# Kernel optimization log

Hardware: AMD Instinct MI355X
Metric: run time of the kernel (lower is better)

## Reference

```python
import jax, jax.numpy as jnp
import numpy as np

B, N, C, H = 16, 577, 768, 12
D = C // H
BETA = 1.0
KEEP_RATIO = 0.5


def setup_inputs() -> dict:
    key = jax.random.key(0)
    k0, k1, k2, k3 = jax.random.split(key, 4)
    x = jax.random.normal(k0, (B, N, C), dtype=jnp.float32)
    # UCB visit-count buffer, strictly positive as accumulated counts would be
    ucb_count_score = jax.random.uniform(k1, (H, N), dtype=jnp.float32) * 50.0 + 1.0
    Wqkv = jax.random.normal(k2, (3 * C, C), dtype=jnp.float32) * 0.02
    Wproj = jax.random.normal(k3, (C, C), dtype=jnp.float32) * 0.02
    bproj = jnp.zeros((C,), dtype=jnp.float32)
    counter = 60  # > 50 so pruning path is taken
    return {"x": x, "ucb_count_score": ucb_count_score, "Wqkv": Wqkv,
            "Wproj": Wproj, "bproj": bproj, "counter": counter}


def reference(x, ucb_count_score, Wqkv, Wproj, bproj, counter):
    # UCBAttention.forward with pruning_enabled=True, selection_mode='ucb',
    # ucb_update_enabled=True, exclude_cls=True, dropout=0 (eval).
    Bs, Ns, Cs = x.shape
    scale = D ** -0.5
    k_keep = max(1, int((Ns - 1) * KEEP_RATIO))  # _get_k with keep_ratio

    qkv = (x @ Wqkv.T).reshape(Bs, Ns, 3, H, D).transpose(2, 0, 3, 1, 4)  # [3,B,H,N,D]
    q, k, v = qkv[0], qkv[1], qkv[2]
    attn_scores = jnp.einsum('bhqd,bhkd->bhqk', q, k) * scale
    attn_probs = jax.nn.softmax(attn_scores, axis=-1)  # [B,H,N,N]

    # UCB scores over patches (CLS excluded)
    patch_scores = attn_probs[:, :, :, 1:].mean(axis=2)            # [B,H,N-1]
    expl = BETA * jnp.sqrt(jnp.log(counter + 1.0) / (ucb_count_score[:, 1:] + 1e-6))
    ucb_scores = patch_scores + expl[None, :, :]                   # [B,H,N-1]
    global_ucb = ucb_scores.mean(axis=1)                           # [B,N-1]
    _, topk_rel = jax.lax.top_k(global_ucb, k_keep)                # [B,k]
    kept = topk_rel + 1                                            # token indices

    # keep-vector: CLS (0) always kept; mask[i,j] = kept[i] OR kept[j]
    kv_mask = (jnp.zeros((Bs, Ns), attn_probs.dtype)
               .at[jnp.arange(Bs)[:, None], kept].set(1.0)
               .at[:, 0].set(1.0))                                 # [B,N]
    mask = jnp.maximum(kv_mask[:, None, :, None], kv_mask[:, None, None, :])  # [B,1,N,N]

    pruned = attn_probs * mask
    pruned = pruned / (pruned.sum(axis=-1, keepdims=True) + 1e-8)
    context = jnp.einsum('bhqk,bhkd->bhqd', pruned, v)             # [B,H,N,D]

    out = context.transpose(0, 2, 1, 3).reshape(Bs, Ns, Cs) @ Wproj.T + bproj

    # score_delta: +1/B at each kept token column, broadcast over heads
    delta = jnp.zeros((Ns,), jnp.float32).at[kept.reshape(-1)].add(1.0 / Bs)
    score_delta = jnp.broadcast_to(delta[None, :], ucb_count_score.shape)
    return out, score_delta, kept
```

## Files before the change

### kernel.cpp

```cpp
#include <hip/hip_runtime.h>
#include <cstdio>
#include <cstdint>

#define B_    16
#define N_    577
#define C_    768
#define H_    12
#define D_    64
#define KKEEP 288
#define SCALE 0.125f
#define LOG2E 1.4426950408889634f
#define M_TOT (B_ * N_)
#define NKT   24
#define PLROW ((size_t)N_ * 64)

typedef __bf16 bf16x8_t __attribute__((ext_vector_type(8)));
typedef __bf16 bf16x4_t __attribute__((ext_vector_type(4)));
typedef float  f32x4_t  __attribute__((ext_vector_type(4)));
typedef unsigned int u32x4_t __attribute__((ext_vector_type(4)));
typedef unsigned int u32x2_t __attribute__((ext_vector_type(2)));

__device__ __forceinline__ f32x4_t mfma_bf16(bf16x8_t a, bf16x8_t b, f32x4_t c) {
    return __builtin_amdgcn_mfma_f32_16x16x32_bf16(a, b, c, 0, 0, 0);
}

__device__ __forceinline__ void gload16(const ushort* g, ushort* l) {
    __builtin_amdgcn_global_load_lds(
        (const __attribute__((address_space(1))) void*)g,
        (__attribute__((address_space(3))) void*)l, 16, 0, 0);
}
#define VMCNT(n) asm volatile("s_waitcnt vmcnt(" #n ")" ::: "memory")
#define LGKM0()  asm volatile("s_waitcnt lgkmcnt(0)" ::: "memory")
#define SB() __builtin_amdgcn_sched_barrier(0)

__device__ __forceinline__ int xcd_swz(int bid, int nwg) {
    int q = nwg >> 3, r = nwg & 7;
    int xcd = bid & 7, off = bid >> 3;
    int base = (xcd < r) ? xcd * (q + 1) : r * (q + 1) + (xcd - r) * q;
    return base + off;
}

__device__ __forceinline__ void splitf(float x, unsigned int &hi, unsigned int &lo) {
    unsigned int u = __float_as_uint(x);
    hi = u >> 16;
    float r = x - __uint_as_float(u & 0xffff0000u);
    lo = __float_as_uint(r) >> 16;
}
__device__ __forceinline__ unsigned int bf16rne(float x) {
    unsigned int u = __float_as_uint(x);
    return (u + 0x7fffu + ((u >> 16) & 1u)) >> 16;
}

__device__ __forceinline__ void pack_tile(const float* __restrict__ src,
                                          ushort* __restrict__ dH,
                                          ushort* __restrict__ dL,
                                          int nrows, int tile) {
    int kt = tile % NKT, mt = tile / NKT;
    int w = threadIdx.x;
    int row = w >> 1, h = w & 1;
    int m = mt * 128 + row;
    int sw = (row >> 1) & 3;
    float f[16];
    if (m < nrows) {
        const float* s = src + (size_t)m * C_ + kt * 32;
        int sa = (2 * h) ^ sw, sb = (2 * h + 1) ^ sw;
        *(float4*)&f[0]  = *(const float4*)(s + sa * 8);
        *(float4*)&f[4]  = *(const float4*)(s + sa * 8 + 4);
        *(float4*)&f[8]  = *(const float4*)(s + sb * 8);
        *(float4*)&f[12] = *(const float4*)(s + sb * 8 + 4);
    } else {
#pragma unroll
        for (int i = 0; i < 16; i++) f[i] = 0.f;
    }
    unsigned hi[16], lo[16];
#pragma unroll
    for (int i = 0; i < 16; i++) splitf(f[i], hi[i], lo[i]);
    u32x4_t h0 = {hi[0] | (hi[1] << 16), hi[2] | (hi[3] << 16),
                  hi[4] | (hi[5] << 16), hi[6] | (hi[7] << 16)};
    u32x4_t h1 = {hi[8] | (hi[9] << 16), hi[10] | (hi[11] << 16),
                  hi[12] | (hi[13] << 16), hi[14] | (hi[15] << 16)};
    u32x4_t l0 = {lo[0] | (lo[1] << 16), lo[2] | (lo[3] << 16),
                  lo[4] | (lo[5] << 16), lo[6] | (lo[7] << 16)};
    u32x4_t l1 = {lo[8] | (lo[9] << 16), lo[10] | (lo[11] << 16),
                  lo[12] | (lo[13] << 16), lo[14] | (lo[15] << 16)};
    size_t dbase = (size_t)tile * 4096 + row * 32;
    *(u32x4_t*)&dH[dbase + (2 * h) * 8]     = h0;
    *(u32x4_t*)&dH[dbase + (2 * h + 1) * 8] = h1;
    *(u32x4_t*)&dL[dbase + (2 * h) * 8]     = l0;
    *(u32x4_t*)&dL[dbase + (2 * h + 1) * 8] = l1;
}

__device__ __forceinline__ void pack_tile_rne(const float* __restrict__ src,
                                              ushort* __restrict__ dst,
                                              int nrows, int tile) {
    int kt = tile % NKT, mt = tile / NKT;
    int w = threadIdx.x;
    int row = w >> 1, h = w & 1;
    int m = mt * 128 + row;
    int sw = (row >> 1) & 3;
    float f[16];
    if (m < nrows) {
        const float* s = src + (size_t)m * C_ + kt * 32;
        int sa = (2 * h) ^ sw, sb = (2 * h + 1) ^ sw;
        *(float4*)&f[0]  = *(const float4*)(s + sa * 8);
        *(float4*)&f[4]  = *(const float4*)(s + sa * 8 + 4);
        *(float4*)&f[8]  = *(const float4*)(s + sb * 8);
        *(float4*)&f[12] = *(const float4*)(s + sb * 8 + 4);
    } else {
#pragma unroll
        for (int i = 0; i < 16; i++) f[i] = 0.f;
    }
    unsigned hi[16];
#pragma unroll
    for (int i = 0; i < 16; i++) hi[i] = bf16rne(f[i]);
    u32x4_t h0 = {hi[0] | (hi[1] << 16), hi[2] | (hi[3] << 16),
                  hi[4] | (hi[5] << 16), hi[6] | (hi[7] << 16)};
    u32x4_t h1 = {hi[8] | (hi[9] << 16), hi[10] | (hi[11] << 16),
                  hi[12] | (hi[13] << 16), hi[14] | (hi[15] << 16)};
    size_t dbase = (size_t)tile * 4096 + row * 32;
    *(u32x4_t*)&dst[dbase + (2 * h) * 8]     = h0;
    *(u32x4_t*)&dst[dbase + (2 * h + 1) * 8] = h1;
}

#define NXP 1752
#define NWP 432
#define NPJ 144
#define NZ  37

__global__ __launch_bounds__(256) void pack_all_kernel(const float* __restrict__ x,
                                                       const float* __restrict__ Wqkv,
                                                       const float* __restrict__ Wproj,
                                                       ushort* __restrict__ XplH,
                                                       ushort* __restrict__ XplL,
                                                       ushort* __restrict__ WplH,
                                                       ushort* __restrict__ WplL,
                                                       ushort* __restrict__ Wpjb,
                                                       float* __restrict__ kvmask) {
    int bid = blockIdx.x;
    if (bid < NXP) {
        pack_tile(x, XplH, XplL, M_TOT, bid);
    } else if (bid < NXP + NWP) {
        pack_tile(Wqkv, WplH, WplL, 3 * C_, bid - NXP);
    } else if (bid < NXP + NWP + NPJ) {
        pack_tile_rne(Wproj, Wpjb, C_, bid - NXP - NWP);
    } else {
        int i = (bid - NXP - NWP - NPJ) * 256 + threadIdx.x;
        if (i < B_ * N_) kvmask[i] = 0.f;
    }
}

__device__ __forceinline__ bf16x8_t fragT(const ushort* H, int row, int c, int ls) {
    int phys = ((c << 2) + ls) ^ (row & 7);
    return __builtin_bit_cast(bf16x8_t, *(const u32x4_t*)&H[(row << 6) + (phys << 3)]);
}

__global__ __launch_bounds__(256) void gemm_qkv_mfma(const ushort* __restrict__ XplH,
                                                     const ushort* __restrict__ XplL,
                                                     const ushort* __restrict__ WplH,
                                                     const ushort* __restrict__ WplL,
                                                     ushort* __restrict__ qhp,
                                                     ushort* __restrict__ qlp,
                                                     ushort* __restrict__ khp,
                                                     ushort* __restrict__ klp,
                                                     ushort* __restrict__ vtp) {
    __shared__ ushort SMEM[32768];
    ushort* Ah = SMEM;
    ushort* Al = SMEM + 8192;
    ushort* Bh = SMEM + 16384;
    ushort* Bl = SMEM + 24576;
    const int bid = xcd_swz(blockIdx.x, 18 * 73);
    const int bx = bid % 18, by = bid / 18;
    const int tid = threadIdx.x;
    const int lane = tid & 63, wave = tid >> 6;
    const int wr = wave >> 1, wc = wave & 1;
    const int lr = lane & 15, ls = lane >> 4;
    const int m0 = by * 128;
    const int o0 = wave * 1024, o1 = o0 + 512;
    const int la = lane * 8;
    const size_t abase = (size_t)by * NKT * 4096;
    const size_t bbase = (size_t)bx * NKT * 4096;
    f32x4_t acc[4][4] = {};

    if (bx < 12) {
        auto stage = [&](int buf, int kt) {
            const size_t ta = abase + (size_t)kt * 4096;
            const size_t tb = bbase + (size_t)kt * 4096;
            gload16(XplH + ta + o0 + la, &Ah[buf * 4096 + o0]);
            gload16(XplH + ta + o1 + la, &Ah[buf * 4096 + o1]);
            gload16(XplL + ta + o0 + la, &Al[buf * 4096 + o0]);
            gload16(XplL + ta + o1 + la, &Al[buf * 4096 + o1]);
            gload16(WplH + tb + o0 + la, &Bh[buf * 4096 + o0]);
            gload16(WplH + tb + o1 + la, &Bh[buf * 4096 + o1]);
            gload16(WplL + tb + o0 + la, &Bl[buf * 4096 + o0]);
            gload16(WplL + tb + o1 + la, &Bl[buf * 4096 + o1]);
        };
        stage(0, 0);
#pragma unroll 1
        for (int kt = 0; kt < NKT; ++kt) {
            const int cur = kt & 1;
            if (kt + 1 < NKT) {
                stage(cur ^ 1, kt + 1);
                VMCNT(8);
            } else {
                VMCNT(0);
            }
            SB();
            __builtin_amdgcn_s_barrier();
            SB();
            bf16x8_t fah[4], fal[4], fbh[4], fbl[4];
#pragma unroll
            for (int i = 0; i < 4; i++) {
                int rowA = wr * 64 + i * 16 + lr;
                int pa = ls ^ ((rowA >> 1) & 3);
                fah[i] = __builtin_bit_cast(bf16x8_t, *(const u32x4_t*)&Ah[cur * 4096 + rowA * 32 + pa * 8]);
                fal[i] = __builtin_bit_cast(bf16x8_t, *(const u32x4_t*)&Al[cur * 4096 + rowA * 32 + pa * 8]);
                int rowB = wc * 64 + i * 16 + lr;
                int pb = ls ^ ((rowB >> 1) & 3);
                fbh[i] = __builtin_bit_cast(bf16x8_t, *(const u32x4_t*)&Bh[cur * 4096 + rowB * 32 + pb * 8]);
                fbl[i] = __builtin_bit_cast(bf16x8_t, *(const u32x4_t*)&Bl[cur * 4096 + rowB * 32 + pb * 8]);
            }
#pragma unroll
            for (int i = 0; i < 4; i++)
#pragma unroll
                for (int j = 0; j < 4; j++) {
                    acc[i][j] = mfma_bf16(fah[i], fbh[j], acc[i][j]);
                    acc[i][j] = mfma_bf16(fah[i], fbl[j], acc[i][j]);
                    acc[i][j] = mfma_bf16(fal[i], fbh[j], acc[i][j]);
                }
            if (kt + 1 < NKT) {
                SB();
                __builtin_amdgcn_s_barrier();
            }
        }
        const int n0 = bx * 128;
        const int s = n0 / C_;
        __syncthreads();
        unsigned* T = (unsigned*)SMEM;
        const float sc = (s == 0) ? SCALE * LOG2E : 1.0f;
#pragma unroll
        for (int j = 0; j < 4; j++) {
            int nl = wc * 64 + j * 16 + lr;
#pragma unroll
            for (int i = 0; i < 4; i++) {
#pragma unroll
                for (int r = 0; r < 4; r++) {
                    int ml = wr * 64 + i * 16 + ls * 4 + r;
                    unsigned hi, lo;
                    splitf(acc[i][j][r] * sc, hi, lo);
                    int idx = ml * 128 + ((((nl >> 3) ^ ((ml >> 2) & 7)) << 3) | (nl & 7));
                    T[idx] = hi | (lo << 16);
                }
            }
        }
        __syncthreads();
        ushort* dh = (s == 1) ? khp : qhp;
        ushort* dl = (s == 1) ? klp : qlp;
        const int hh0 = (n0 % C_) / D_;
#pragma unroll
        for (int it = 0; it < 8; ++it) {
            int g = it * 256 + tid;
            int sl = g & 7;
            int m_local = (g >> 3) & 127;
            int hh_half = g >> 10;
            int m = m0 + m_local;
            if (m < M_TOT) {
                int b = m / N_, n = m % N_;
                int dg = sl ^ (n & 7);
                int grp = (hh_half * 8 + dg) ^ ((m_local >> 2) & 7);
                const unsigned* src = &T[m_local * 128 + grp * 8];
                u32x4_t a = *(const u32x4_t*)src;
                u32x4_t bvv = *(const u32x4_t*)(src + 4);
                u32x4_t hiv = {(a[0] & 0xffffu) | (a[1] << 16),
                               (a[2] & 0xffffu) | (a[3] << 16),
                               (bvv[0] & 0xffffu) | (bvv[1] << 16),
                               (bvv[2] & 0xffffu) | (bvv[3] << 16)};
                u32x4_t lov = {(a[0] >> 16) | (a[1] & 0xffff0000u),
                               (a[2] >> 16) | (a[3] & 0xffff0000u),
                               (bvv[0] >> 16) | (bvv[1] & 0xffff0000u),
                               (bvv[2] >> 16) | (bvv[3] & 0xffff0000u)};
                size_t off = (size_t)(b * H_ + hh0 + hh_half) * PLROW + (size_t)n * 64 + sl * 8;
                *(u32x4_t*)&dh[off] = hiv;
                *(u32x4_t*)&dl[off] = lov;
            }
        }
    } else {
        auto stage = [&](int buf, int kt) {
            const size_t ta = abase + (size_t)kt * 4096;
            const size_t tb = bbase + (size_t)kt * 4096;
            gload16(XplH + ta + o0 + la, &Ah[buf * 4096 + o0]);
            gload16(XplH + ta + o1 + la, &Ah[buf * 4096 + o1]);
            gload16(XplL + ta + o0 + la, &Al[buf * 4096 + o0]);
            gload16(XplL + ta + o1 + la, &Al[buf * 4096 + o1]);
            gload16(WplH + tb + o0 + la, &Bh[buf * 4096 + o0]);
            gload16(WplH + tb + o1 + la, &Bh[buf * 4096 + o1]);
        };
        stage(0, 0);
#pragma unroll 1
        for (int kt = 0; kt < NKT; ++kt) {
            const int cur = kt & 1;
            if (kt + 1 < NKT) {
                stage(cur ^ 1, kt + 1);
                VMCNT(6);
            } else {
                VMCNT(0);
            }
            SB();
            __builtin_amdgcn_s_barrier();
            SB();
            bf16x8_t fah[4], fal[4], fbh[4];
#pragma unroll
            for (int i = 0; i < 4; i++) {
                int rowA = wr * 64 + i * 16 + lr;
                int pa = ls ^ ((rowA >> 1) & 3);
                fah[i] = __builtin_bit_cast(bf16x8_t, *(const u32x4_t*)&Ah[cur * 4096 + rowA * 32 + pa * 8]);
                fal[i] = __builtin_bit_cast(bf16x8_t, *(const u32x4_t*)&Al[cur * 4096 + rowA * 32 + pa * 8]);
                int rowB = wc * 64 + i * 16 + lr;
                int pb = ls ^ ((rowB >> 1) & 3);
                fbh[i] = __builtin_bit_cast(bf16x8_t, *(const u32x4_t*)&Bh[cur * 4096 + rowB * 32 + pb * 8]);
            }
#pragma unroll
            for (int i = 0; i < 4; i++)
#pragma unroll
                for (int j = 0; j < 4; j++) {
                    acc[i][j] = mfma_bf16(fah[i], fbh[j], acc[i][j]);
                    acc[i][j] = mfma_bf16(fal[i], fbh[j], acc[i][j]);
                }
            if (kt + 1 < NKT) {
                SB();
                __builtin_amdgcn_s_barrier();
            }
        }
        const int n0v = (bx - 12) * 128;
#pragma unroll
        for (int j = 0; j < 4; j++) {
            int ng = n0v + wc * 64 + j * 16 + lr;
            int hh = ng / D_;
            int d = ng % D_;
#pragma unroll
            for (int i = 0; i < 4; i++) {
                int mg0 = m0 + wr * 64 + i * 16 + ls * 4;
#pragma unroll
                for (int r = 0; r < 4; r++) {
                    int m = mg0 + r;
                    if (m < M_TOT) {
                        int b = m / N_, n = m % N_;
                        int jt = n >> 6, jl = n & 63;
                        size_t off = ((size_t)(b * H_ + hh) * 10 + jt) * 4096 +
                                     (size_t)d * 64 + (((jl >> 3) ^ (d & 7)) << 3) + (jl & 7);
                        vtp[off] = __builtin_bit_cast(unsigned short, (__bf16)acc[i][j][r]);
                    }
                }
            }
        }
    }
}

__global__ __launch_bounds__(512) void attn_rowsum_mfma(const ushort* __restrict__ qh,
                                                        const ushort* __restrict__ ql,
                                                        const ushort* __restrict__ kh,
                                                        const ushort* __restrict__ kl,
                                                        float* __restrict__ w) {
    __shared__ ushort Qh[8192], Ql[8192];
    __shared__ ushort Kh[4096], Kl[4096];
    __shared__ float red[8][64];
    const int bid = xcd_swz(blockIdx.x, 5 * B_ * H_);
    const int bh = bid / 5, q0 = (bid % 5) * 128;
    const int tid = threadIdx.x, lane = tid & 63, wv = tid >> 6;
    const int wg = wv >> 2, wl = wv & 3;
    const int lr = lane & 15, ls = lane >> 4;
    const size_t bho = (size_t)bh * PLROW;
    const ushort* qhp = qh + bho; const ushort* qlp = ql + bho;
    const ushort* khp = kh + bho; const ushort* klp = kl + bho;
    auto qrow = [&](int rr) { return (size_t)min(q0 + wv * 16 + rr * 8 + (lane >> 3), N_ - 1) * 64 + (lane & 7) * 8; };
    gload16(qhp + qrow(0), &Qh[wv * 1024]);
    gload16(qhp + qrow(1), &Qh[wv * 1024 + 512]);
    gload16(qlp + qrow(0), &Ql[wv * 1024]);
    gload16(qlp + qrow(1), &Ql[wv * 1024 + 512]);
    auto krow = [&](int j0) { return (size_t)min(j0 + wv * 8 + (lane >> 3), N_ - 1) * 64 + (lane & 7) * 8; };
    auto stageK = [&](int j0) {
        gload16(khp + krow(j0), &Kh[wv * 512]);
        gload16(klp + krow(j0), &Kl[wv * 512]);
    };
    stageK(0);
    VMCNT(0);
    __syncthreads();
    bf16x8_t fqh[4][2], fql[4][2];
#pragma unroll
    for (int i = 0; i < 4; i++)
#pragma unroll
        for (int c = 0; c < 2; c++) {
            fqh[i][c] = fragT(Qh, wg * 64 + i * 16 + lr, c, ls);
            fql[i][c] = fragT(Ql, wg * 64 + i * 16 + lr, c, ls);
        }
    float rs[4] = {0.f, 0.f, 0.f, 0.f};
#pragma unroll 1
    for (int t = 0; t < 10; ++t) {
        bf16x8_t fkh[2], fkl[2];
#pragma unroll
        for (int c = 0; c < 2; c++) {
            fkh[c] = fragT(Kh, wl * 16 + lr, c, ls);
            fkl[c] = fragT(Kl, wl * 16 + lr, c, ls);
        }
        LGKM0(); SB();
        __builtin_amdgcn_s_barrier();
        SB();
        if (t < 9) stageK((t + 1) * 64);
        int jbase = t * 64 + wl * 16 + ls * 4;
#pragma unroll
        for (int i = 0; i < 4; i++) {
            f32x4_t s = {0.f, 0.f, 0.f, 0.f};
            __builtin_amdgcn_s_setprio(1);
#pragma unroll
            for (int c = 0; c < 2; c++) {
                s = mfma_bf16(fkh[c], fqh[i][c], s);
                s = mfma_bf16(fkh[c], fql[i][c], s);
                s = mfma_bf16(fkl[c], fqh[i][c], s);
            }
            __builtin_amdgcn_s_setprio(0);
#pragma unroll
            for (int r = 0; r < 4; r++)
                rs[i] += (jbase + r < N_) ? __builtin_amdgcn_exp2f(s[r]) : 0.f;
        }
        if (t < 9) {
            VMCNT(0); SB();
            __builtin_amdgcn_s_barrier();
            SB();
        }
    }
#pragma unroll
    for (int i = 0; i < 4; i++) {
        float v2 = rs[i];
        v2 += __shfl_xor(v2, 16);
        v2 += __shfl_xor(v2, 32);
        if (ls == 0) red[wv][i * 16 + lr] = v2;
    }
    __syncthreads();
    if (tid < 128) {
        int grp = tid >> 6, qlc = tid & 63;
        float s = red[grp * 4 + 0][qlc] + red[grp * 4 + 1][qlc] +
                  red[grp * 4 + 2][qlc] + red[grp * 4 + 3][qlc];
        int qn = q0 + tid;
        if (qn < N_) w[(size_t)bh * N_ + qn] = 1.0f / s;
    }
}

__global__ __launch_bounds__(512) void attn_colsum_mfma(const ushort* __restrict__ qh,
                                                        const ushort* __restrict__ ql,
                                                        const ushort* __restrict__ kh,
                                                        const ushort* __restrict__ kl,
                                                        const float* __restrict__ w,
                                                        float* __restrict__ colsum) {
    __shared__ ushort KhS[8192], KlS[8192];
    __shared__ ushort Qh[4096], Ql[4096];
    __shared__ float wsAll[640];
    __shared__ float red[8][64];
    const int bid = xcd_swz(blockIdx.x, 5 * B_ * H_);
    const int bh = bid / 5, j0 = (bid % 5) * 128;
    const int tid = threadIdx.x, lane = tid & 63, wv = tid >> 6;
    const int wg = wv >> 2, wl = wv & 3;
    const int lr = lane & 15, ls = lane >> 4;
    const size_t bho = (size_t)bh * PLROW;
    const ushort* qhp = qh + bho; const ushort* qlp = ql + bho;
    const ushort* khp = kh + bho; const ushort* klp = kl + bho;
    auto krow = [&](int rr) { return (size_t)min(j0 + wv * 16 + rr * 8 + (lane >> 3), N_ - 1) * 64 + (lane & 7) * 8; };
    gload16(khp + krow(0), &KhS[wv * 1024]);
    gload16(khp + krow(1), &KhS[wv * 1024 + 512]);
    gload16(klp + krow(0), &KlS[wv * 1024]);
    gload16(klp + krow(1), &KlS[wv * 1024 + 512]);
    auto qrow2 = [&](int qt) { return (size_t)min(qt + wv * 8 + (lane >> 3), N_ - 1) * 64 + (lane & 7) * 8; };
    auto stageQ = [&](int qt) {
        gload16(qhp + qrow2(qt), &Qh[wv * 512]);
        gload16(qlp + qrow2(qt), &Ql[wv * 512]);
    };
    stageQ(0);
    for (int i2 = tid; i2 < 640; i2 += 512)
        wsAll[i2] = (i2 < N_) ? w[(size_t)bh * N_ + i2] : 0.f;
    VMCNT(0);
    __syncthreads();
    bf16x8_t fkh[4][2], fkl[4][2];
#pragma unroll
    for (int i = 0; i < 4; i++)
#pragma unroll
        for (int c = 0; c < 2; c++) {
            fkh[i][c] = fragT(KhS, wg * 64 + i * 16 + lr, c, ls);
            fkl[i][c] = fragT(KlS, wg * 64 + i * 16 + lr, c, ls);
        }
    float cs[4] = {0.f, 0.f, 0.f, 0.f};
#pragma unroll 1
    for (int t = 0; t < 10; ++t) {
        bf16x8_t fqh[2], fql[2];
#pragma unroll
        for (int c = 0; c < 2; c++) {
            fqh[c] = fragT(Qh, wl * 16 + lr, c, ls);
            fql[c] = fragT(Ql, wl * 16 + lr, c, ls);
        }
        float wq[4];
#pragma unroll
        for (int r = 0; r < 4; r++) wq[r] = wsAll[t * 64 + wl * 16 + ls * 4 + r];
        LGKM0(); SB();
        __builtin_amdgcn_s_barrier();
        SB();
        if (t < 9) stageQ((t + 1) * 64);
#pragma unroll
        for (int i = 0; i < 4; i++) {
            f32x4_t s = {0.f, 0.f, 0.f, 0.f};
            __builtin_amdgcn_s_setprio(1);
#pragma unroll
            for (int c = 0; c < 2; c++) {
                s = mfma_bf16(fqh[c], fkh[i][c], s);
                s = mfma_bf16(fql[c], fkh[i][c], s);
                s = mfma_bf16(fqh[c], fkl[i][c], s);
            }
            __builtin_amdgcn_s_setprio(0);
#pragma unroll
            for (int r = 0; r < 4; r++) cs[i] += __builtin_amdgcn_exp2f(s[r]) * wq[r];
        }
        if (t < 9) {
            VMCNT(0); SB();
            __builtin_amdgcn_s_barrier();
            SB();
        }
    }
#pragma unroll
    for (int i = 0; i < 4; i++) {
        float v2 = cs[i];
        v2 += __shfl_xor(v2, 16);
        v2 += __shfl_xor(v2, 32);
        if (ls == 0) red[wv][i * 16 + lr] = v2;
    }
    __syncthreads();
    if (tid < 128) {
        int grp = tid >> 6, jlc = tid & 63;
        float t2 = red[grp * 4 + 0][jlc] + red[grp * 4 + 1][jlc] +
                   red[grp * 4 + 2][jlc] + red[grp * 4 + 3][jlc];
        int jn = j0 + tid;
        if (jn < N_) colsum[(size_t)bh * N_ + jn] = t2;
    }
}

__global__ __launch_bounds__(512) void topk_kernel(const float* __restrict__ colsum,
                                                   const float* __restrict__ ucb_count,
                                                   const int* __restrict__ counter,
                                                   float* __restrict__ kept_out,
                                                   float* __restrict__ kvmask) {
    __shared__ float sv[1024];
    __shared__ int si[1024];
    int b = blockIdx.x, tid = threadIdx.x;
    float lc = logf((float)counter[0] + 1.0f);
    for (int t = tid; t < 1024; t += 512) {
        if (t < N_ - 1) {
            int tok = t + 1;
            float accv = 0.f;
#pragma unroll
            for (int h = 0; h < H_; h++) {
                float csv = colsum[(size_t)(b * H_ + h) * N_ + tok];
                float patch = csv * (1.0f / (float)N_);
                float cnt = ucb_count[h * N_ + tok];
                float expl = sqrtf(lc / (cnt + 1e-6f));
                accv += patch + expl;
            }
            sv[t] = accv * (1.0f / (float)H_);
            si[t] = t;
        } else {
            sv[t] = -INFINITY;
            si[t] = 1 << 20;
        }
    }
    __syncthreads();
    for (int kk = 2; kk <= 1024; kk <<= 1) {
        for (int jj = kk >> 1; jj > 0; jj >>= 1) {
            for (int t = tid; t < 1024; t += 512) {
                int ixj = t ^ jj;
                if (ixj > t) {
                    float v1 = sv[t], v2 = sv[ixj];
                    int i1 = si[t], i2 = si[ixj];
                    bool before21 = (v2 > v1) || (v2 == v1 && i2 < i1);
                    bool dirDesc = ((t & kk) == 0);
                    if (before21 == dirDesc) {
                        sv[t] = v2; sv[ixj] = v1;
                        si[t] = i2; si[ixj] = i1;
                    }
                }
            }
            __syncthreads();
        }
    }
    for (int r = tid; r < KKEEP; r += 512) {
        int tok = si[r] + 1;
        kept_out[b * KKEEP + r] = (float)tok;
        kvmask[b * N_ + tok] = 1.0f;
    }
    if (tid == 0) kvmask[b * N_] = 1.0f;
}

__global__ __launch_bounds__(512) void attn_ctx_mfma(const ushort* __restrict__ qh,
                                                     const ushort* __restrict__ ql,
                                                     const ushort* __restrict__ kh,
                                                     const ushort* __restrict__ vtp,
                                                     const float* __restrict__ kvmask,
                                                     ushort* __restrict__ ctxb,
                                                     float* __restrict__ sd) {
    if (blockIdx.x >= 5 * B_ * H_) {
        int idx = (blockIdx.x - 5 * B_ * H_) * 512 + threadIdx.x;
        if (idx < H_ * N_) {
            int n = idx % N_;
            float d = 0.f;
            if (n != 0) {
#pragma unroll
                for (int b = 0; b < B_; b++) d += kvmask[b * N_ + n];
            }
            sd[idx] = d * (1.0f / (float)B_);
        }
        return;
    }
    __shared__ ushort Kh[2][4096], Vt[2][4096];
    __shared__ ushort Pl[2][4096];
    __shared__ float mkAll[640];
    float (*red)[64] = (float(*)[64])&Pl[0][0];
    float* inv = (float*)&Pl[1][0];
    const int bid = xcd_swz(blockIdx.x, 5 * B_ * H_);
    const int bh = bid / 5, q0 = (bid % 5) * 128;
    const int b = bh / H_, h = bh % H_;
    const int tid = threadIdx.x, lane = tid & 63, wv = tid >> 6;
    const int wg = wv >> 2, wl = wv & 3;
    const int lr = lane & 15, ls = lane >> 4;
    const size_t bho = (size_t)bh * PLROW;
    const ushort* qhp = qh + bho; const ushort* qlp = ql + bho;
    const ushort* khp = kh + bho;
    const ushort* vtb = vtp + (size_t)bh * 10 * 4096;
    ushort* PlS = &Pl[0][0];
    for (int i2 = tid; i2 < 640; i2 += 512)
        mkAll[i2] = (i2 < N_) ? kvmask[(size_t)b * N_ + i2] : 0.f;
    auto qrow = [&](int rr) { return (size_t)min(q0 + wv * 16 + rr * 8 + (lane >> 3), N_ - 1) * 64 + (lane & 7) * 8; };
    bf16x8_t fqh[4][2], fql[4][2];
    gload16(qhp + qrow(0), &PlS[wv * 1024]);
    gload16(qhp + qrow(1), &PlS[wv * 1024 + 512]);
    VMCNT(0); __syncthreads();
#pragma unroll
    for (int i = 0; i < 4; i++)
#pragma unroll
        for (int c = 0; c < 2; c++)
            fqh[i][c] = fragT(PlS, wg * 64 + i * 16 + lr, c, ls);
    __syncthreads();
    gload16(qlp + qrow(0), &PlS[wv * 1024]);
    gload16(qlp + qrow(1), &PlS[wv * 1024 + 512]);
    VMCNT(0); __syncthreads();
#pragma unroll
    for (int i = 0; i < 4; i++)
#pragma unroll
        for (int c = 0; c < 2; c++)
            fql[i][c] = fragT(PlS, wg * 64 + i * 16 + lr, c, ls);
    __syncthreads();
    auto krow = [&](int j0) { return (size_t)min(j0 + wv * 8 + (lane >> 3), N_ - 1) * 64 + (lane & 7) * 8; };
    auto stageKV = [&](int buf, int t) {
        gload16(khp + krow(t * 64), &Kh[buf][wv * 512]);
        gload16(vtb + (size_t)t * 4096 + wv * 512 + lane * 8, &Vt[buf][wv * 512]);
    };
    float mq[4];
#pragma unroll
    for (int i = 0; i < 4; i++) mq[i] = mkAll[q0 + wg * 64 + i * 16 + lr];
    stageKV(0, 0);
    f32x4_t acc[4] = {};
    float psums[4] = {0.f, 0.f, 0.f, 0.f};
#pragma unroll 1
    for (int t = 0; t < 10; ++t) {
        const int cur = t & 1;
        if (t < 9) { stageKV(cur ^ 1, t + 1); VMCNT(2); }
        else      { VMCNT(0); }
        SB(); __builtin_amdgcn_s_barrier(); SB();
        bf16x8_t fkh[2];
#pragma unroll
        for (int c = 0; c < 2; c++)
            fkh[c] = fragT(Kh[cur], wl * 16 + lr, c, ls);
        int jloc = wl * 16 + ls * 4;
        float jmv[4], jbias[4];
#pragma unroll
        for (int r = 0; r < 4; r++) {
            int j = t * 64 + jloc + r;
            jmv[r] = mkAll[t * 64 + jloc + r];
            jbias[r] = (j < N_) ? 0.f : -16384.f;
        }
#pragma unroll
        for (int i = 0; i < 4; i++) {
            f32x4_t s = {0.f, 0.f, 0.f, 0.f};
            __builtin_amdgcn_s_setprio(1);
#pragma unroll
            for (int c = 0; c < 2; c++) {
                s = mfma_bf16(fkh[c], fqh[i][c], s);
                s = mfma_bf16(fkh[c], fql[i][c], s);
            }
            __builtin_amdgcn_s_setprio(0);
            bf16x4_t pb;
            float mqi = mq[i];
#pragma unroll
            for (int r = 0; r < 4; r++) {
                float p = __builtin_amdgcn_exp2f(s[r] + jbias[r]) * fmaxf(mqi, jmv[r]);
                psums[i] += p;
                pb[r] = (__bf16)p;
            }
            int row = i * 16 + lr;
            int slot = ((wl << 1) + (ls >> 1)) ^ (row & 7);
            *(u32x2_t*)&Pl[wg][(row << 6) + (slot << 3) + ((ls & 1) << 2)] =
                __builtin_bit_cast(u32x2_t, pb);
        }
        SB(); LGKM0(); SB();
        __builtin_amdgcn_s_barrier();
        SB();
        bf16x8_t fv[2];
#pragma unroll
        for (int c = 0; c < 2; c++) fv[c] = fragT(Vt[cur], wl * 16 + lr, c, ls);
        __builtin_amdgcn_s_setprio(1);
#pragma unroll
        for (int i = 0; i < 4; i++) {
            bf16x8_t fp0 = fragT(Pl[wg], i * 16 + lr, 0, ls);
            bf16x8_t fp1 = fragT(Pl[wg], i * 16 + lr, 1, ls);
            acc[i] = mfma_bf16(fv[0], fp0, acc[i]);
            acc[i] = mfma_bf16(fv[1], fp1, acc[i]);
        }
        __builtin_amdgcn_s_setprio(0);
        if (t < 9) { SB(); __builtin_amdgcn_s_barrier(); }
    }
    __syncthreads();
#pragma unroll
    for (int i = 0; i < 4; i++) {
        float v2 = psums[i];
        v2 += __shfl_xor(v2, 16);
        v2 += __shfl_xor(v2, 32);
        if (ls == 0) red[wv][i * 16 + lr] = v2;
    }
    __syncthreads();
    if (tid < 128) {
        int grp = tid >> 6, qlc = tid & 63;
        float t2 = red[grp * 4 + 0][qlc] + red[grp * 4 + 1][qlc] +
                   red[grp * 4 + 2][qlc] + red[grp * 4 + 3][qlc];
        inv[tid] = 1.0f / (t2 + 1e-8f);
    }
    __syncthreads();
#pragma unroll
    for (int i = 0; i < 4; i++) {
        int qn = q0 + wg * 64 + i * 16 + lr;
        if (qn < N_) {
            float rn = inv[wg * 64 + i * 16 + lr];
            bf16x4_t ov;
            ov[0] = (__bf16)(acc[i][0] * rn);
            ov[1] = (__bf16)(acc[i][1] * rn);
            ov[2] = (__bf16)(acc[i][2] * rn);
            ov[3] = (__bf16)(acc[i][3] * rn);
            int m = b * N_ + qn;
            int col = h * D_ + wl * 16 + ls * 4;
            int mt = m >> 7, rowl = m & 127;
            int kt2 = col >> 5, c32 = col & 31;
            int phys = (c32 >> 3) ^ ((rowl >> 1) & 3);
            size_t off = ((size_t)(mt * NKT + kt2)) * 4096 + rowl * 32 + phys * 8 + (c32 & 7);
            *(u32x2_t*)&ctxb[off] = __builtin_bit_cast(u32x2_t, ov);
        }
    }
}

__global__ __launch_bounds__(256) void gemm_proj_mfma(const ushort* __restrict__ Apl,
                                                      const ushort* __restrict__ Bpl,
                                                      const float* __restrict__ bias,
                                                      float* __restrict__ out) {
    __shared__ ushort Ab[2][4096], Bb[2][4096];
    const int bid = xcd_swz(blockIdx.x, 6 * 73);
    const int bx = bid % 6, by = bid / 6;
    const int tid = threadIdx.x;
    const int lane = tid & 63, wave = tid >> 6;
    const int wr = wave >> 1, wc = wave & 1;
    const int lr = lane & 15, ls = lane >> 4;
    const int m0 = by * 128, n0 = bx * 128;
    const int o0 = wave * 1024, o1 = o0 + 512;
    const int la = lane * 8;
    const size_t abase = (size_t)by * NKT * 4096;
    const size_t bbase = (size_t)bx * NKT * 4096;
    f32x4_t acc[4][4] = {};

    auto stage = [&](int buf, int kt) {
        const size_t ta = abase + (size_t)kt * 4096;
        const size_t tb = bbase + (size_t)kt * 4096;
        gload16(Apl + ta + o0 + la, &Ab[buf][o0]);
        gload16(Apl + ta + o1 + la, &Ab[buf][o1]);
        gload16(Bpl + tb + o0 + la, &Bb[buf][o0]);
        gload16(Bpl + tb + o1 + la, &Bb[buf][o1]);
    };
    stage(0, 0);
#pragma unroll 1
    for (int kt = 0; kt < NKT; ++kt) {
        const int cur = kt & 1;
        if (kt + 1 < NKT) {
            stage(cur ^ 1, kt + 1);
            VMCNT(4);
        } else {
            VMCNT(0);
        }
        SB();
        __builtin_amdgcn_s_barrier();
        SB();
        bf16x8_t fa[4], fb[4];
#pragma unroll
        for (int i = 0; i < 4; i++) {
            int rowA = wr * 64 + i * 16 + lr;
            int pa = ls ^ ((rowA >> 1) & 3);
            fa[i] = __builtin_bit_cast(bf16x8_t, *(const u32x4_t*)&Ab[cur][rowA * 32 + pa * 8]);
            int rowB = wc * 64 + i * 16 + lr;
            int pb = ls ^ ((rowB >> 1) & 3);
            fb[i] = __builtin_bit_cast(bf16x8_t, *(const u32x4_t*)&Bb[cur][rowB * 32 + pb * 8]);
        }
#pragma unroll
        for (int i = 0; i < 4; i++)
#pragma unroll
            for (int j = 0; j < 4; j++)
                acc[i][j] = mfma_bf16(fa[i], fb[j], acc[i][j]);
        if (kt + 1 < NKT) {
            SB();
            __builtin_amdgcn_s_barrier();
        }
    }
#pragma unroll
    for (int j = 0; j < 4; j++) {
        int ng = n0 + wc * 64 + j * 16 + lr;
        float bb = bias[ng];
#pragma unroll
        for (int i = 0; i < 4; i++) {
            int mg0 = m0 + wr * 64 + i * 16 + ls * 4;
#pragma unroll
            for (int r = 0; r < 4; r++) {
                int m = mg0 + r;
                if (m < M_TOT) out[(size_t)m * C_ + ng] = acc[i][j][r] + bb;
            }
        }
    }
}

extern "C" void kernel_launch(void* const* d_in, const int* in_sizes, int n_in,
                              void* d_out, int out_size, void* d_ws, size_t ws_size,
                              hipStream_t stream) {
    const float* x     = (const float*)d_in[0];
    const float* ucb   = (const float*)d_in[1];
    const float* Wqkv  = (const float*)d_in[2];
    const float* Wproj = (const float*)d_in[3];
    const float* bproj = (const float*)d_in[4];
    const int*   counter = (const int*)d_in[5];

    const size_t BHN  = (size_t)B_ * H_ * N_;
    const size_t XPL  = (size_t)(73 * 128) * C_;
    const size_t WPL  = (size_t)3 * C_ * C_;
    const size_t WPJ  = (size_t)C_ * C_;
    const size_t PLN  = (size_t)192 * PLROW;
    const size_t VTSZ = (size_t)192 * 10 * 4096;

    ushort* qhp  = (ushort*)d_ws;
    ushort* qlp  = qhp + PLN;
    ushort* khp  = qlp + PLN;
    ushort* klp  = khp + PLN;
    ushort* vtp  = klp + PLN;
    ushort* XplH = vtp + VTSZ;
    ushort* XplL = XplH + XPL;
    ushort* ctxb = XplH;
    ushort* WplH = XplL + XPL;
    ushort* WplL = WplH + WPL;
    ushort* Wpjb = WplL + WPL;
    float*  w    = (float*)(Wpjb + WPJ);
    float*  colsum = w + BHN;
    float*  kvmask = colsum + BHN;
    size_t need = ((char*)(kvmask + (size_t)B_ * N_)) - (char*)d_ws;
    if (ws_size < need) {
        fprintf(stderr, "kernel_launch: ws too small, need %zu have %zu\n",
                need, ws_size);
        return;
    }

    float* out  = (float*)d_out;
    float* sd   = out + (size_t)B_ * N_ * C_;
    float* kept = sd + (size_t)H_ * N_;

    pack_all_kernel<<<NXP + NWP + NPJ + NZ, 256, 0, stream>>>(
        x, Wqkv, Wproj, XplH, XplL, WplH, WplL, Wpjb, kvmask);

    gemm_qkv_mfma<<<18 * 73, 256, 0, stream>>>(XplH, XplL, WplH, WplL,
                                               qhp, qlp, khp, klp, vtp);
    attn_rowsum_mfma<<<5 * B_ * H_, 512, 0, stream>>>(qhp, qlp, khp, klp, w);
    attn_colsum_mfma<<<5 * B_ * H_, 512, 0, stream>>>(qhp, qlp, khp, klp, w, colsum);
    topk_kernel<<<B_, 512, 0, stream>>>(colsum, ucb, counter, kept, kvmask);
    attn_ctx_mfma<<<5 * B_ * H_ + 14, 512, 0, stream>>>(qhp, qlp, khp, vtp,
                                                        kvmask, ctxb, sd);
    gemm_proj_mfma<<<6 * 73, 256, 0, stream>>>(ctxb, Wpjb, bproj, out);
}
```

Baseline: 282.6 us.

## Single-buffer QKV GEMM and attention KV tiles to cut LDS usage

Removes double-buffering of the A/B tiles in the QKV projection GEMM, halving its shared memory from 64KB to 32KB. The epilogue now writes hi and lo halves in two rounds through a 16-bit staging buffer. In the attention kernel, the K and V^T tiles are single-buffered too: fragments are read into registers first, then the next tile is prefetched while compute proceeds. The aim is more resident blocks per CU, at the cost of losing load/compute overlap in the GEMM, which now waits on VMCNT(0) every k-step.

```diff
diff --git a/kernel.cpp b/kernel.cpp
--- a/kernel.cpp
+++ b/kernel.cpp
@@ -163,11 +163,11 @@
                                                      ushort* __restrict__ khp,
                                                      ushort* __restrict__ klp,
                                                      ushort* __restrict__ vtp) {
-    __shared__ ushort SMEM[32768];
+    __shared__ ushort SMEM[16384];
     ushort* Ah = SMEM;
-    ushort* Al = SMEM + 8192;
-    ushort* Bh = SMEM + 16384;
-    ushort* Bl = SMEM + 24576;
+    ushort* Al = SMEM + 4096;
+    ushort* Bh = SMEM + 8192;
+    ushort* Bl = SMEM + 12288;
     const int bid = xcd_swz(blockIdx.x, 18 * 73);
     const int bx = bid % 18, by = bid / 18;
     const int tid = threadIdx.x;
@@ -175,35 +175,29 @@
     const int wr = wave >> 1, wc = wave & 1;
     const int lr = lane & 15, ls = lane >> 4;
     const int m0 = by * 128;
-    const int o0 = wave * 1024, o1 = o0 + 512;
+    const int ow = wave * 1024;
     const int la = lane * 8;
     const size_t abase = (size_t)by * NKT * 4096;
     const size_t bbase = (size_t)bx * NKT * 4096;
     f32x4_t acc[4][4] = {};
 
     if (bx < 12) {
-        auto stage = [&](int buf, int kt) {
+        auto stage = [&](int kt) {
             const size_t ta = abase + (size_t)kt * 4096;
             const size_t tb = bbase + (size_t)kt * 4096;
-            gload16(XplH + ta + o0 + la, &Ah[buf * 4096 + o0]);
-            gload16(XplH + ta + o1 + la, &Ah[buf * 4096 + o1]);
-            gload16(XplL + ta + o0 + la, &Al[buf * 4096 + o0]);
-            gload16(XplL + ta + o1 + la, &Al[buf * 4096 + o1]);
-            gload16(WplH + tb + o0 + la, &Bh[buf * 4096 + o0]);
-            gload16(WplH + tb + o1 + la, &Bh[buf * 4096 + o1]);
-            gload16(WplL + tb + o0 + la, &Bl[buf * 4096 + o0]);
-            gload16(WplL + tb + o1 + la, &Bl[buf * 4096 + o1]);
+            gload16(XplH + ta + ow + la, &Ah[ow]);
+            gload16(XplH + ta + ow + 512 + la, &Ah[ow + 512]);
+            gload16(XplL + ta + ow + la, &Al[ow]);
+            gload16(XplL + ta + ow + 512 + la, &Al[ow + 512]);
+            gload16(WplH + tb + ow + la, &Bh[ow]);
+            gload16(WplH + tb + ow + 512 + la, &Bh[ow + 512]);
+            gload16(WplL + tb + ow + la, &Bl[ow]);
+            gload16(WplL + tb + ow + 512 + la, &Bl[ow + 512]);
         };
-        stage(0, 0);
 #pragma unroll 1
         for (int kt = 0; kt < NKT; ++kt) {
-            const int cur = kt & 1;
-            if (kt + 1 < NKT) {
-                stage(cur ^ 1, kt + 1);
-                VMCNT(8);
-            } else {
-                VMCNT(0);
-            }
+            stage(kt);
+            VMCNT(0);
             SB();
             __builtin_amdgcn_s_barrier();
             SB();
@@ -212,12 +206,12 @@
             for (int i = 0; i < 4; i++) {
                 int rowA = wr * 64 + i * 16 + lr;
                 int pa = ls ^ ((rowA >> 1) & 3);
-                fah[i] = __builtin_bit_cast(bf16x8_t, *(const u32x4_t*)&Ah[cur * 4096 + rowA * 32 + pa * 8]);
-                fal[i] = __builtin_bit_cast(bf16x8_t, *(const u32x4_t*)&Al[cur * 4096 + rowA * 32 + pa * 8]);
+                fah[i] = __builtin_bit_cast(bf16x8_t, *(const u32x4_t*)&Ah[rowA * 32 + pa * 8]);
+                fal[i] = __builtin_bit_cast(bf16x8_t, *(const u32x4_t*)&Al[rowA * 32 + pa * 8]);
                 int rowB = wc * 64 + i * 16 + lr;
                 int pb = ls ^ ((rowB >> 1) & 3);
-                fbh[i] = __builtin_bit_cast(bf16x8_t, *(const u32x4_t*)&Bh[cur * 4096 + rowB * 32 + pb * 8]);
-                fbl[i] = __builtin_bit_cast(bf16x8_t, *(const u32x4_t*)&Bl[cur * 4096 + rowB * 32 + pb * 8]);
+                fbh[i] = __builtin_bit_cast(bf16x8_t, *(const u32x4_t*)&Bh[rowB * 32 + pb * 8]);
+                fbl[i] = __builtin_bit_cast(bf16x8_t, *(const u32x4_t*)&Bl[rowB * 32 + pb * 8]);
             }
 #pragma unroll
             for (int i = 0; i < 4; i++)
@@ -227,83 +221,68 @@
                     acc[i][j] = mfma_bf16(fah[i], fbl[j], acc[i][j]);
                     acc[i][j] = mfma_bf16(fal[i], fbh[j], acc[i][j]);
                 }
-            if (kt + 1 < NKT) {
-                SB();
-                __builtin_amdgcn_s_barrier();
-            }
+            SB();
+            __builtin_amdgcn_s_barrier();
         }
         const int n0 = bx * 128;
         const int s = n0 / C_;
-        __syncthreads();
-        unsigned* T = (unsigned*)SMEM;
         const float sc = (s == 0) ? SCALE * LOG2E : 1.0f;
-#pragma unroll
-        for (int j = 0; j < 4; j++) {
-            int nl = wc * 64 + j * 16 + lr;
-#pragma unroll
-            for (int i = 0; i < 4; i++) {
-#pragma unroll
-                for (int r = 0; r < 4; r++) {
-                    int ml = wr * 64 + i * 16 + ls * 4 + r;
-                    unsigned hi, lo;
-                    splitf(acc[i][j][r] * sc, hi, lo);
-                    int idx = ml * 128 + ((((nl >> 3) ^ ((ml >> 2) & 7)) << 3) | (nl & 7));
-                    T[idx] = hi | (lo << 16);
-                }
-            }
-        }
-        __syncthreads();
         ushort* dh = (s == 1) ? khp : qhp;
         ushort* dl = (s == 1) ? klp : qlp;
         const int hh0 = (n0 % C_) / D_;
-#pragma unroll
-        for (int it = 0; it < 8; ++it) {
-            int g = it * 256 + tid;
-            int sl = g & 7;
-            int m_local = (g >> 3) & 127;
-            int hh_half = g >> 10;
-            int m = m0 + m_local;
-            if (m < M_TOT) {
-                int b = m / N_, n = m % N_;
-                int dg = sl ^ (n & 7);
-                int grp = (hh_half * 8 + dg) ^ ((m_local >> 2) & 7);
-                const unsigned* src = &T[m_local * 128 + grp * 8];
-                u32x4_t a = *(const u32x4_t*)src;
-                u32x4_t bvv = *(const u32x4_t*)(src + 4);
-                u32x4_t hiv = {(a[0] & 0xffffu) | (a[1] << 16),
-                               (a[2] & 0xffffu) | (a[3] << 16),
-                               (bvv[0] & 0xffffu) | (bvv[1] << 16),
-                               (bvv[2] & 0xffffu) | (bvv[3] << 16)};
-                u32x4_t lov = {(a[0] >> 16) | (a[1] & 0xffff0000u),
-                               (a[2] >> 16) | (a[3] & 0xffff0000u),
-                               (bvv[0] >> 16) | (bvv[1] & 0xffff0000u),
-                               (bvv[2] >> 16) | (bvv[3] & 0xffff0000u)};
-                size_t off = (size_t)(b * H_ + hh0 + hh_half) * PLROW + (size_t)n * 64 + sl * 8;
-                *(u32x4_t*)&dh[off] = hiv;
-                *(u32x4_t*)&dl[off] = lov;
-            }
+        ushort* T16 = SMEM;
+#pragma unroll 1
+        for (int round = 0; round < 2; ++round) {
+#pragma unroll
+            for (int j = 0; j < 4; j++) {
+                int nl = wc * 64 + j * 16 + lr;
+#pragma unroll
+                for (int i = 0; i < 4; i++) {
+#pragma unroll
+                    for (int r = 0; r < 4; r++) {
+                        int ml = wr * 64 + i * 16 + ls * 4 + r;
+                        unsigned hi, lo;
+                        splitf(acc[i][j][r] * sc, hi, lo);
+                        int idx = ml * 128 + ((((nl >> 3) ^ ((ml >> 2) & 7)) << 3) | (nl & 7));
+                        T16[idx] = (ushort)(round ? lo : hi);
+                    }
+                }
+            }
+            __syncthreads();
+            ushort* dst = round ? dl : dh;
+#pragma unroll
+            for (int it = 0; it < 8; ++it) {
+                int g = it * 256 + tid;
+                int sl = g & 7;
+                int m_local = (g >> 3) & 127;
+                int hh_half = g >> 10;
+                int m = m0 + m_local;
+                if (m < M_TOT) {
+                    int b = m / N_, n = m % N_;
+                    int dg = sl ^ (n & 7);
+                    int grp = (hh_half * 8 + dg) ^ ((m_local >> 2) & 7);
+                    u32x4_t vv = *(const u32x4_t*)&T16[m_local * 128 + grp * 8];
+                    size_t off = (size_t)(b * H_ + hh0 + hh_half) * PLROW + (size_t)n * 64 + sl * 8;
+                    *(u32x4_t*)&dst[off] = vv;
+                }
+            }
+            if (round == 0) __syncthreads();
         }
     } else {
-        auto stage = [&](int buf, int kt) {
+        auto stage = [&](int kt) {
             const size_t ta = abase + (size_t)kt * 4096;
             const size_t tb = bbase + (size_t)kt * 4096;
-            gload16(XplH + ta + o0 + la, &Ah[buf * 4096 + o0]);
-            gload16(XplH + ta + o1 + la, &Ah[buf * 4096 + o1]);
-            gload16(XplL + ta + o0 + la, &Al[buf * 4096 + o0]);
-            gload16(XplL + ta + o1 + la, &Al[buf * 4096 + o1]);
-            gload16(WplH + tb + o0 + la, &Bh[buf * 4096 + o0]);
-            gload16(WplH + tb + o1 + la, &Bh[buf * 4096 + o1]);
+            gload16(XplH + ta + ow + la, &Ah[ow]);
+            gload16(XplH + ta + ow + 512 + la, &Ah[ow + 512]);
+            gload16(XplL + ta + ow + la, &Al[ow]);
+            gload16(XplL + ta + ow + 512 + la, &Al[ow + 512]);
+            gload16(WplH + tb + ow + la, &Bh[ow]);
+            gload16(WplH + tb + ow + 512 + la, &Bh[ow + 512]);
         };
-        stage(0, 0);
 #pragma unroll 1
         for (int kt = 0; kt < NKT; ++kt) {
-            const int cur = kt & 1;
-            if (kt + 1 < NKT) {
-                stage(cur ^ 1, kt + 1);
-                VMCNT(6);
-            } else {
-                VMCNT(0);
-            }
+            stage(kt);
+            VMCNT(0);
             SB();
             __builtin_amdgcn_s_barrier();
             SB();
@@ -312,11 +291,11 @@
             for (int i = 0; i < 4; i++) {
                 int rowA = wr * 64 + i * 16 + lr;
                 int pa = ls ^ ((rowA >> 1) & 3);
-                fah[i] = __builtin_bit_cast(bf16x8_t, *(const u32x4_t*)&Ah[cur * 4096 + rowA * 32 + pa * 8]);
-                fal[i] = __builtin_bit_cast(bf16x8_t, *(const u32x4_t*)&Al[cur * 4096 + rowA * 32 + pa * 8]);
+                fah[i] = __builtin_bit_cast(bf16x8_t, *(const u32x4_t*)&Ah[rowA * 32 + pa * 8]);
+                fal[i] = __builtin_bit_cast(bf16x8_t, *(const u32x4_t*)&Al[rowA * 32 + pa * 8]);
                 int rowB = wc * 64 + i * 16 + lr;
                 int pb = ls ^ ((rowB >> 1) & 3);
-                fbh[i] = __builtin_bit_cast(bf16x8_t, *(const u32x4_t*)&Bh[cur * 4096 + rowB * 32 + pb * 8]);
+                fbh[i] = __builtin_bit_cast(bf16x8_t, *(const u32x4_t*)&Bh[rowB * 32 + pb * 8]);
             }
 #pragma unroll
             for (int i = 0; i < 4; i++)
@@ -325,10 +304,8 @@
                     acc[i][j] = mfma_bf16(fah[i], fbh[j], acc[i][j]);
                     acc[i][j] = mfma_bf16(fal[i], fbh[j], acc[i][j]);
                 }
-            if (kt + 1 < NKT) {
-                SB();
-                __builtin_amdgcn_s_barrier();
-            }
+            SB();
+            __builtin_amdgcn_s_barrier();
         }
         const int n0v = (bx - 12) * 128;
 #pragma unroll
@@ -613,7 +590,7 @@
         }
         return;
     }
-    __shared__ ushort Kh[2][4096], Vt[2][4096];
+    __shared__ ushort Kh[4096], Vt[4096];
     __shared__ ushort Pl[2][4096];
     __shared__ float mkAll[640];
     float (*red)[64] = (float(*)[64])&Pl[0][0];
@@ -652,26 +629,30 @@
             fql[i][c] = fragT(PlS, wg * 64 + i * 16 + lr, c, ls);
     __syncthreads();
     auto krow = [&](int j0) { return (size_t)min(j0 + wv * 8 + (lane >> 3), N_ - 1) * 64 + (lane & 7) * 8; };
-    auto stageKV = [&](int buf, int t) {
-        gload16(khp + krow(t * 64), &Kh[buf][wv * 512]);
-        gload16(vtb + (size_t)t * 4096 + wv * 512 + lane * 8, &Vt[buf][wv * 512]);
+    auto stageKV = [&](int t) {
+        gload16(khp + krow(t * 64), &Kh[wv * 512]);
+        gload16(vtb + (size_t)t * 4096 + wv * 512 + lane * 8, &Vt[wv * 512]);
     };
     float mq[4];
 #pragma unroll
     for (int i = 0; i < 4; i++) mq[i] = mkAll[q0 + wg * 64 + i * 16 + lr];
-    stageKV(0, 0);
+    stageKV(0);
+    VMCNT(0);
+    SB(); __builtin_amdgcn_s_barrier(); SB();
     f32x4_t acc[4] = {};
     float psums[4] = {0.f, 0.f, 0.f, 0.f};
 #pragma unroll 1
     for (int t = 0; t < 10; ++t) {
-        const int cur = t & 1;
-        if (t < 9) { stageKV(cur ^ 1, t + 1); VMCNT(2); }
-        else      { VMCNT(0); }
-        SB(); __builtin_amdgcn_s_barrier(); SB();
-        bf16x8_t fkh[2];
-#pragma unroll
-        for (int c = 0; c < 2; c++)
-            fkh[c] = fragT(Kh[cur], wl * 16 + lr, c, ls);
+        bf16x8_t fkh[2], fv[2];
+#pragma unroll
+        for (int c = 0; c < 2; c++) {
+            fkh[c] = fragT(Kh, wl * 16 + lr, c, ls);
+            fv[c]  = fragT(Vt, wl * 16 + lr, c, ls);
+        }
+        LGKM0(); SB();
+        __builtin_amdgcn_s_barrier();
+        SB();
+        if (t < 9) stageKV(t + 1);
         int jloc = wl * 16 + ls * 4;
         float jmv[4], jbias[4];
 #pragma unroll
@@ -706,9 +687,6 @@
         SB(); LGKM0(); SB();
         __builtin_amdgcn_s_barrier();
         SB();
-        bf16x8_t fv[2];
-#pragma unroll
-        for (int c = 0; c < 2; c++) fv[c] = fragT(Vt[cur], wl * 16 + lr, c, ls);
         __builtin_amdgcn_s_setprio(1);
 #pragma unroll
         for (int i = 0; i < 4; i++) {
@@ -718,7 +696,11 @@
             acc[i] = mfma_bf16(fv[1], fp1, acc[i]);
         }
         __builtin_amdgcn_s_setprio(0);
-        if (t < 9) { SB(); __builtin_amdgcn_s_barrier(); }
+        if (t < 9) {
+            VMCNT(0); SB();
+            __builtin_amdgcn_s_barrier();
+            SB();
+        }
     }
     __syncthreads();
 #pragma unroll
```

After: 275.7 us. 1.03x faster.
